# Kernel optimization log

Hardware: AMD Instinct MI355X
Metric: run time of the kernel (lower is better)

## Reference

```python
import jax, jax.numpy as jnp
import numpy as np

N_NODES = 50000
N_EDGES = 800000
F_IN = 512
H1 = 64
H2 = 128
N_CLASSES = 10
N_GRAPHS = 64


def _sage_conv(x, src, dst, w_l, b_l, w_r, n_nodes):
    # mean-aggregate neighbor features (messages flow src -> dst), then
    # out = lin_l(mean_neigh) + lin_r(x)   (PyG SAGEConv defaults)
    msg = x[src]                                           # [E, F] gather
    agg = jax.ops.segment_sum(msg, dst, num_segments=n_nodes)
    deg = jax.ops.segment_sum(jnp.ones((src.shape[0], 1), x.dtype), dst,
                              num_segments=n_nodes)
    mean = agg / jnp.maximum(deg, 1.0)                     # 0 for isolated nodes
    return mean @ w_l + b_l + x @ w_r


def setup_inputs() -> dict:
    key = jax.random.key(0)
    ks = jax.random.split(key, 12)
    x = jax.random.normal(ks[0], (N_NODES, F_IN), dtype=jnp.float32)
    edge_index = jax.random.randint(ks[1], (2, N_EDGES), 0, N_NODES, dtype=jnp.int64)
    batch = jnp.sort(jax.random.randint(ks[2], (N_NODES,), 0, N_GRAPHS, dtype=jnp.int64))

    def glorot(k, fan_in, fan_out):
        s = jnp.sqrt(6.0 / (fan_in + fan_out)).astype(jnp.float32)
        return jax.random.uniform(k, (fan_in, fan_out), jnp.float32, -s, s)

    return {
        "x": x, "edge_index": edge_index, "batch": batch,
        "w1_l": glorot(ks[3], F_IN, H1), "b1_l": jnp.zeros((H1,), jnp.float32),
        "w1_r": glorot(ks[4], F_IN, H1),
        "w2_l": glorot(ks[5], H1, H2), "b2_l": jnp.zeros((H2,), jnp.float32),
        "w2_r": glorot(ks[6], H1, H2),
        "w_fc": glorot(ks[7], H2, N_CLASSES),
        "b_fc": jnp.zeros((N_CLASSES,), jnp.float32),
    }


def reference(x, edge_index, batch, w1_l, b1_l, w1_r, w2_l, b2_l, w2_r, w_fc, b_fc):
    src, dst = edge_index[0], edge_index[1]
    n = x.shape[0]
    h = jax.nn.relu(_sage_conv(x, src, dst, w1_l, b1_l, w1_r, n))
    # dropout is identity in eval mode
    h = _sage_conv(h, src, dst, w2_l, b2_l, w2_r, n)        # [N, H2]
    # global mean pool over graphs
    summed = jax.ops.segment_sum(h, batch, num_segments=N_GRAPHS)
    cnt = jax.ops.segment_sum(jnp.ones((n, 1), h.dtype), batch, num_segments=N_GRAPHS)
    pooled = summed / jnp.maximum(cnt, 1.0)                 # [G, H2]
    logits = pooled @ w_fc + b_fc                           # [G, C]
    return jax.nn.log_softmax(logits, axis=1)
```

## Files before the change

kernel.cpp:

```cpp
#include <hip/hip_runtime.h>

#define NN 50000
#define NE 800000
#define FIN 512
#define H1DIM 64
#define H2DIM 128
#define NC 10
#define NG 64
#define NRT 3125
#define SCAN_BLOCKS 196
#define SLICES 8
#define SLICE_NODES (NN / SLICES)
#define SCAT_GRPS 98
#define SCAT_BLOCKS (SLICES * SCAT_GRPS)

typedef __attribute__((ext_vector_type(8))) short bf16x8;
typedef __attribute__((ext_vector_type(4))) float f32x4;

__device__ inline short f2bf(float f) {
  unsigned u = __float_as_uint(f);
  unsigned r = u + 0x7fffu + ((u >> 16) & 1u);
  return (short)(r >> 16);
}
__device__ inline short f2bf_fast(float f) {
  return (short)((__float_as_uint(f) + 0x8000u) >> 16);
}
__device__ inline float bf2f(short s) {
  return __uint_as_float(((unsigned)(unsigned short)s) << 16);
}

__global__ __launch_bounds__(256) void hist_kernel(const int* __restrict__ dst,
                                                   int* __restrict__ cnt) {
  int i = (blockIdx.x * 256 + threadIdx.x) * 4;
  if (i < NE) {
    int4 d = *(const int4*)(dst + i);
    atomicAdd(&cnt[d.x], 1);
    atomicAdd(&cnt[d.y], 1);
    atomicAdd(&cnt[d.z], 1);
    atomicAdd(&cnt[d.w], 1);
  }
}

__global__ __launch_bounds__(256) void scan1_kernel(const int* __restrict__ cnt,
                                                    int* __restrict__ excl,
                                                    int* __restrict__ bsum) {
  __shared__ int s[256];
  int t = threadIdx.x;
  int i = blockIdx.x * 256 + t;
  int v = (i < NN) ? cnt[i] : 0;
  s[t] = v;
  __syncthreads();
  for (int off = 1; off < 256; off <<= 1) {
    int u = (t >= off) ? s[t - off] : 0;
    __syncthreads();
    s[t] += u;
    __syncthreads();
  }
  if (i < NN) excl[i] = s[t] - v;
  if (t == 255) bsum[blockIdx.x] = s[255];
}

__global__ __launch_bounds__(256) void scan23_kernel(const int* __restrict__ bsum,
                                                     int* __restrict__ rowptr,
                                                     int* __restrict__ cursor) {
  __shared__ int s[256];
  int t = threadIdx.x;
  int b = blockIdx.x;
  int v = (t < SCAN_BLOCKS) ? bsum[t] : 0;
  s[t] = v;
  __syncthreads();
  for (int off = 1; off < 256; off <<= 1) {
    int u = (t >= off) ? s[t - off] : 0;
    __syncthreads();
    s[t] += u;
    __syncthreads();
  }
  int prefix = (b == 0) ? 0 : s[b - 1];
  int i = b * 256 + t;
  if (i < NN) {
    int p = rowptr[i] + prefix;
    rowptr[i] = p;
    cursor[i] = p;
  }
  if (i == 0) rowptr[NN] = NE;
}

__global__ __launch_bounds__(256) void scatter_kernel(
    const int* __restrict__ src, const int* __restrict__ dst,
    int* __restrict__ cursor, int* __restrict__ ssrc) {
  int slice = blockIdx.x & 7;
  int lo = slice * SLICE_NODES;
  int hi = lo + SLICE_NODES;
  int tid = (blockIdx.x >> 3) * 256 + threadIdx.x;
  for (int j = tid; j < NE / 4; j += SCAT_GRPS * 256) {
    int4 s = *(const int4*)(src + j * 4);
    int4 d = *(const int4*)(dst + j * 4);
    if (d.x >= lo && d.x < hi) { int p = atomicAdd(&cursor[d.x], 1); ssrc[p] = s.x; }
    if (d.y >= lo && d.y < hi) { int p = atomicAdd(&cursor[d.y], 1); ssrc[p] = s.y; }
    if (d.z >= lo && d.z < hi) { int p = atomicAdd(&cursor[d.z], 1); ssrc[p] = s.z; }
    if (d.w >= lo && d.w < hi) { int p = atomicAdd(&cursor[d.w], 1); ssrc[p] = s.w; }
  }
}

__global__ __launch_bounds__(256) void wbtf_prep_kernel(
    const float* __restrict__ wl, const float* __restrict__ wr,
    short* __restrict__ wbtf) {
  int w = blockIdx.x * 4 + (threadIdx.x >> 6);
  int lane = threadIdx.x & 63;
  int ni = w >> 4;
  int ks = w & 15;
  int n = ni * 16 + (lane & 15);
  int k = ks * 32 + (lane >> 4) * 8;
  bf16x8 o;
#pragma unroll
  for (int j = 0; j < 8; j++) {
    float v = (n < 64) ? wl[(size_t)(k + j) * 64 + n]
                       : wr[(size_t)(k + j) * 64 + (n - 64)];
    o[j] = f2bf(v);
  }
  *(bf16x8*)(wbtf + ((size_t)w * 64 + lane) * 8) = o;
}

__global__ __launch_bounds__(256) void gemm1_kernel(
    const float* __restrict__ x, const short* __restrict__ wbtf,
    short* __restrict__ xwl, float* __restrict__ xwr) {
  __shared__ short Bs[32768];

  const int t = threadIdx.x;
  const int w = blockIdx.x * 4 + (t >> 6);
  const int wc = (w < NRT) ? w : (NRT - 1);
  const int lane = t & 63;
  const int l15 = lane & 15;
  const int q = lane >> 4;
  const float* px = x + (size_t)(wc * 16 + l15) * FIN + q * 8;

  const f32x4 z = {0.f, 0.f, 0.f, 0.f};
  f32x4 acc[8];
#pragma unroll
  for (int ni = 0; ni < 8; ni++) acc[ni] = z;

  float4 ra0[4], ra1[4];
#pragma unroll
  for (int i = 0; i < 4; i++) {
    ra0[i] = *(const float4*)(px + i * 32);
    ra1[i] = *(const float4*)(px + i * 32 + 4);
  }

#pragma unroll
  for (int h = 0; h < 2; h++) {
    if (h > 0) __syncthreads();
#pragma unroll
    for (int i = 0; i < 16; i++) {
      int c = i * 256 + t;
      int ni = c >> 9;
      int rem = c & 511;
      ((bf16x8*)Bs)[c] =
          *(const bf16x8*)(wbtf + (size_t)ni * 8192 + h * 4096 + rem * 8);
    }
    __syncthreads();

#pragma unroll
    for (int ksl = 0; ksl < 8; ksl++) {
      int ks = h * 8 + ksl;
      int slot = ks & 3;
      bf16x8 af;
      {
        float4 v0 = ra0[slot], v1 = ra1[slot];
        af[0] = f2bf_fast(v0.x); af[1] = f2bf_fast(v0.y);
        af[2] = f2bf_fast(v0.z); af[3] = f2bf_fast(v0.w);
        af[4] = f2bf_fast(v1.x); af[5] = f2bf_fast(v1.y);
        af[6] = f2bf_fast(v1.z); af[7] = f2bf_fast(v1.w);
      }
      if (ks + 4 < 16) {
        ra0[slot] = *(const float4*)(px + (ks + 4) * 32);
        ra1[slot] = *(const float4*)(px + (ks + 4) * 32 + 4);
      }
#pragma unroll
      for (int ni = 0; ni < 8; ni++) {
        bf16x8 bf = *(const bf16x8*)(&Bs[((ni * 8 + ksl) * 64 + lane) * 8]);
        acc[ni] = __builtin_amdgcn_mfma_f32_16x16x32_bf16(af, bf, acc[ni], 0, 0, 0);
      }
    }
  }

  int row_base = wc * 16 + q * 4;
#pragma unroll
  for (int ni = 0; ni < 8; ni++) {
    int col = ni * 16 + l15;
    int c = col & 63;
#pragma unroll
    for (int r = 0; r < 4; r++) {
      int row = row_base + r;
      if (col < 64) xwl[(size_t)row * 64 + c] = f2bf(acc[ni][r]);
      else          xwr[(size_t)row * 64 + c] = acc[ni][r];
    }
  }
}

__global__ __launch_bounds__(256) void agg1_h1_kernel(
    const int* __restrict__ rowptr, const int* __restrict__ ssrc,
    const short* __restrict__ xwl, const float* __restrict__ xwr,
    const float* __restrict__ b1, short* __restrict__ h1) {
  int node = blockIdx.x * 4 + (threadIdx.x >> 6);
  if (node >= NN) return;
  int lane = threadIdx.x & 63;
  int c = lane & 7;
  int r = lane >> 3;
  int lo = rowptr[node], hi = rowptr[node + 1];
  float acc[8];
#pragma unroll
  for (int k = 0; k < 8; k++) acc[k] = 0.f;
  for (int e = lo + r; e < hi; e += 8) {
    int s = ssrc[e];
    bf16x8 v = *(const bf16x8*)(xwl + (size_t)s * 64 + c * 8);
#pragma unroll
    for (int k = 0; k < 8; k++) acc[k] += bf2f(v[k]);
  }
#pragma unroll
  for (int k = 0; k < 8; k++) {
    acc[k] += __shfl_xor(acc[k], 8);
    acc[k] += __shfl_xor(acc[k], 16);
    acc[k] += __shfl_xor(acc[k], 32);
  }
  if (r == 0) {
    float dg = fmaxf((float)(hi - lo), 1.0f);
    const float* xr = xwr + (size_t)node * 64 + c * 8;
    bf16x8 out;
#pragma unroll
    for (int k = 0; k < 8; k++) {
      float v = fmaxf(acc[k] / dg + b1[c * 8 + k] + xr[k], 0.f);
      out[k] = f2bf(v);
    }
    *(bf16x8*)(h1 + (size_t)node * 64 + c * 8) = out;
  }
}

__global__ __launch_bounds__(256) void agg2_kernel(
    const int* __restrict__ rowptr, const int* __restrict__ ssrc,
    const short* __restrict__ h1, float* __restrict__ agg2) {
  int node = blockIdx.x * 4 + (threadIdx.x >> 6);
  if (node >= NN) return;
  int lane = threadIdx.x & 63;
  int c = lane & 7;
  int r = lane >> 3;
  int lo = rowptr[node], hi = rowptr[node + 1];
  float acc[8];
#pragma unroll
  for (int k = 0; k < 8; k++) acc[k] = 0.f;
  for (int e = lo + r; e < hi; e += 8) {
    int s = ssrc[e];
    bf16x8 v = *(const bf16x8*)(h1 + (size_t)s * 64 + c * 8);
#pragma unroll
    for (int k = 0; k < 8; k++) acc[k] += bf2f(v[k]);
  }
#pragma unroll
  for (int k = 0; k < 8; k++) {
    acc[k] += __shfl_xor(acc[k], 8);
    acc[k] += __shfl_xor(acc[k], 16);
    acc[k] += __shfl_xor(acc[k], 32);
  }
  if (r == 0) {
    float* p = agg2 + (size_t)node * 64 + c * 8;
    f32x4 lo4 = {acc[0], acc[1], acc[2], acc[3]};
    f32x4 hi4 = {acc[4], acc[5], acc[6], acc[7]};
    *(f32x4*)(p) = lo4;
    *(f32x4*)(p + 4) = hi4;
  }
}

__global__ __launch_bounds__(256) void pool1_kernel(
    const int* __restrict__ batch, const float* __restrict__ agg2,
    const short* __restrict__ h1, const int* __restrict__ rowptr,
    float* __restrict__ poolA, float* __restrict__ poolB,
    float* __restrict__ poolCnt) {
  int t = threadIdx.x;
  int c = t & 15;
  int s = t >> 4;
  int n0 = blockIdx.x * 256 + s * 16;
  int n1 = n0 + 16;
  if (n1 > NN) n1 = NN;

  f32x4 aA = {0.f, 0.f, 0.f, 0.f};
  f32x4 aB = {0.f, 0.f, 0.f, 0.f};
  int cur_g = -1;
  float run = 0.f;
  for (int n = n0; n < n1; n++) {
    int g = batch[n];
    if (g != cur_g) {
      if (cur_g >= 0) {
        float* pa = poolA + (size_t)cur_g * 64 + c * 4;
        float* pb = poolB + (size_t)cur_g * 64 + c * 4;
#pragma unroll
        for (int k = 0; k < 4; k++) {
          atomicAdd(&pa[k], aA[k]);
          atomicAdd(&pb[k], aB[k]);
        }
        if (c == 0) atomicAdd(&poolCnt[cur_g], run);
      }
      cur_g = g;
      aA = (f32x4){0.f, 0.f, 0.f, 0.f};
      aB = (f32x4){0.f, 0.f, 0.f, 0.f};
      run = 0.f;
    }
    float rd = 1.0f / fmaxf((float)(rowptr[n + 1] - rowptr[n]), 1.0f);
    f32x4 a2 = *(const f32x4*)(agg2 + (size_t)n * 64 + c * 4);
    const short* hp = h1 + (size_t)n * 64 + c * 4;
#pragma unroll
    for (int k = 0; k < 4; k++) {
      aA[k] = fmaf(a2[k], rd, aA[k]);
      aB[k] += bf2f(hp[k]);
    }
    run += 1.f;
  }
  if (cur_g >= 0) {
    float* pa = poolA + (size_t)cur_g * 64 + c * 4;
    float* pb = poolB + (size_t)cur_g * 64 + c * 4;
#pragma unroll
    for (int k = 0; k < 4; k++) {
      atomicAdd(&pa[k], aA[k]);
      atomicAdd(&pb[k], aB[k]);
    }
    if (c == 0) atomicAdd(&poolCnt[cur_g], run);
  }
}

__global__ __launch_bounds__(128) void final_kernel(
    const float* __restrict__ poolA, const float* __restrict__ poolB,
    const float* __restrict__ poolCnt, const float* __restrict__ w2l,
    const float* __restrict__ w2r, const float* __restrict__ b2,
    const float* __restrict__ wfc, const float* __restrict__ bfc,
    float* __restrict__ out) {
  int g = blockIdx.x;
  int j = threadIdx.x;
  __shared__ float sp[H2DIM];
  __shared__ float sl[NC];

  float invc = 1.0f / fmaxf(poolCnt[g], 1.0f);
  float v = b2[j];
  for (int k = 0; k < 64; k++) {
    float a = poolA[g * 64 + k] * invc;
    float b = poolB[g * 64 + k] * invc;
    v = fmaf(a, w2l[k * 128 + j], v);
    v = fmaf(b, w2r[k * 128 + j], v);
  }
  sp[j] = v;
  __syncthreads();
  if (j < NC) {
    float lg = bfc[j];
    for (int k = 0; k < H2DIM; k++) lg = fmaf(sp[k], wfc[k * NC + j], lg);
    sl[j] = lg;
  }
  __syncthreads();
  if (j < NC) {
    float m = -1e30f;
    for (int k = 0; k < NC; k++) m = fmaxf(m, sl[k]);
    float s = 0.f;
    for (int k = 0; k < NC; k++) s += expf(sl[k] - m);
    out[g * NC + j] = sl[j] - m - logf(s);
  }
}

extern "C" void kernel_launch(void* const* d_in, const int* in_sizes, int n_in,
                              void* d_out, int out_size, void* d_ws,
                              size_t ws_size, hipStream_t stream) {
  const float* x   = (const float*)d_in[0];
  const int* edge  = (const int*)d_in[1];
  const int* batch = (const int*)d_in[2];
  const float* w1l = (const float*)d_in[3];
  const float* b1l = (const float*)d_in[4];
  const float* w1r = (const float*)d_in[5];
  const float* w2l = (const float*)d_in[6];
  const float* b2l = (const float*)d_in[7];
  const float* w2r = (const float*)d_in[8];
  const float* wfc = (const float*)d_in[9];
  const float* bfc = (const float*)d_in[10];
  float* out = (float*)d_out;

  const int* src = edge;
  const int* dst = edge + NE;

  const size_t NF = (size_t)NN * 64;
  int*   cnt     = (int*)d_ws;
  float* poolA   = (float*)(cnt + NN);
  float* poolB   = poolA + (size_t)NG * 64;
  float* poolCnt = poolB + (size_t)NG * 64;
  int*   cursor  = (int*)(poolCnt + NG);
  int*   rowptr  = cursor + NN;
  int*   bsum    = rowptr + 50004;
  int*   ssrc    = bsum + 256;
  short* xwl     = (short*)(ssrc + NE);
  short* h1s     = xwl + NF;
  short* wbtf    = h1s + NF;
  float* xwr     = (float*)(wbtf + 65536);
  float* agg2    = xwr + NF;

  hipMemsetAsync(cnt, 0, (NN + 2 * NG * 64 + NG) * sizeof(int), stream);

  hist_kernel<<<(NE / 4 + 255) / 256, 256, 0, stream>>>(dst, cnt);
  scan1_kernel<<<SCAN_BLOCKS, 256, 0, stream>>>(cnt, rowptr, bsum);
  scan23_kernel<<<SCAN_BLOCKS, 256, 0, stream>>>(bsum, rowptr, cursor);
  scatter_kernel<<<SCAT_BLOCKS, 256, 0, stream>>>(src, dst, cursor, ssrc);

  wbtf_prep_kernel<<<32, 256, 0, stream>>>(w1l, w1r, wbtf);
  gemm1_kernel<<<(NRT + 3) / 4, 256, 0, stream>>>(x, wbtf, xwl, xwr);

  agg1_h1_kernel<<<(NN + 3) / 4, 256, 0, stream>>>(rowptr, ssrc, xwl, xwr, b1l, h1s);
  agg2_kernel<<<(NN + 3) / 4, 256, 0, stream>>>(rowptr, ssrc, h1s, agg2);
  pool1_kernel<<<SCAN_BLOCKS, 256, 0, stream>>>(batch, agg2, h1s, rowptr, poolA, poolB, poolCnt);
  final_kernel<<<NG, 128, 0, stream>>>(poolA, poolB, poolCnt, w2l, w2r, b2l, wfc, bfc, out);
}
```

Baseline: 351.3 us.

## Merge independent kernels into horizontally fused launches to overlap scatter with GEMM

Folds the weight-prep kernel into the histogram launch as extra blocks, and merges the CSR scatter with the first GEMM into one launch whose blocks branch by block index. The aim is to cut launch count and let the latency-bound atomic scatter overlap with the compute-bound GEMM on the same device. In exchange, scatter blocks now reserve the GEMM's 64KB of shared memory, which may reduce how many scatter blocks fit on a CU at once.

```diff
diff --git a/kernel.cpp b/kernel.cpp
--- a/kernel.cpp
+++ b/kernel.cpp
@@ -13,6 +13,8 @@
 #define SLICE_NODES (NN / SLICES)
 #define SCAT_GRPS 98
 #define SCAT_BLOCKS (SLICES * SCAT_GRPS)
+#define HIST_BLOCKS 782
+#define GEMM_BLOCKS 782
 
 typedef __attribute__((ext_vector_type(8))) short bf16x8;
 typedef __attribute__((ext_vector_type(4))) float f32x4;
@@ -29,15 +31,35 @@
   return __uint_as_float(((unsigned)(unsigned short)s) << 16);
 }
 
-__global__ __launch_bounds__(256) void hist_kernel(const int* __restrict__ dst,
-                                                   int* __restrict__ cnt) {
-  int i = (blockIdx.x * 256 + threadIdx.x) * 4;
-  if (i < NE) {
-    int4 d = *(const int4*)(dst + i);
-    atomicAdd(&cnt[d.x], 1);
-    atomicAdd(&cnt[d.y], 1);
-    atomicAdd(&cnt[d.z], 1);
-    atomicAdd(&cnt[d.w], 1);
+__global__ __launch_bounds__(256) void histwbtf_kernel(
+    const int* __restrict__ dst, int* __restrict__ cnt,
+    const float* __restrict__ wl, const float* __restrict__ wr,
+    short* __restrict__ wbtf) {
+  int b = blockIdx.x;
+  if (b < HIST_BLOCKS) {
+    int i = (b * 256 + threadIdx.x) * 4;
+    if (i < NE) {
+      int4 d = *(const int4*)(dst + i);
+      atomicAdd(&cnt[d.x], 1);
+      atomicAdd(&cnt[d.y], 1);
+      atomicAdd(&cnt[d.z], 1);
+      atomicAdd(&cnt[d.w], 1);
+    }
+  } else {
+    int w = (b - HIST_BLOCKS) * 4 + (threadIdx.x >> 6);
+    int lane = threadIdx.x & 63;
+    int ni = w >> 4;
+    int ks = w & 15;
+    int n = ni * 16 + (lane & 15);
+    int k = ks * 32 + (lane >> 4) * 8;
+    bf16x8 o;
+#pragma unroll
+    for (int j = 0; j < 8; j++) {
+      float v = (n < 64) ? wl[(size_t)(k + j) * 64 + n]
+                         : wr[(size_t)(k + j) * 64 + (n - 64)];
+      o[j] = f2bf(v);
+    }
+    *(bf16x8*)(wbtf + ((size_t)w * 64 + lane) * 8) = o;
   }
 }
 
@@ -85,49 +107,31 @@
   if (i == 0) rowptr[NN] = NE;
 }
 
-__global__ __launch_bounds__(256) void scatter_kernel(
+__global__ __launch_bounds__(256) void scatgemm_kernel(
     const int* __restrict__ src, const int* __restrict__ dst,
-    int* __restrict__ cursor, int* __restrict__ ssrc) {
-  int slice = blockIdx.x & 7;
-  int lo = slice * SLICE_NODES;
-  int hi = lo + SLICE_NODES;
-  int tid = (blockIdx.x >> 3) * 256 + threadIdx.x;
-  for (int j = tid; j < NE / 4; j += SCAT_GRPS * 256) {
-    int4 s = *(const int4*)(src + j * 4);
-    int4 d = *(const int4*)(dst + j * 4);
-    if (d.x >= lo && d.x < hi) { int p = atomicAdd(&cursor[d.x], 1); ssrc[p] = s.x; }
-    if (d.y >= lo && d.y < hi) { int p = atomicAdd(&cursor[d.y], 1); ssrc[p] = s.y; }
-    if (d.z >= lo && d.z < hi) { int p = atomicAdd(&cursor[d.z], 1); ssrc[p] = s.z; }
-    if (d.w >= lo && d.w < hi) { int p = atomicAdd(&cursor[d.w], 1); ssrc[p] = s.w; }
-  }
-}
-
-__global__ __launch_bounds__(256) void wbtf_prep_kernel(
-    const float* __restrict__ wl, const float* __restrict__ wr,
-    short* __restrict__ wbtf) {
-  int w = blockIdx.x * 4 + (threadIdx.x >> 6);
-  int lane = threadIdx.x & 63;
-  int ni = w >> 4;
-  int ks = w & 15;
-  int n = ni * 16 + (lane & 15);
-  int k = ks * 32 + (lane >> 4) * 8;
-  bf16x8 o;
-#pragma unroll
-  for (int j = 0; j < 8; j++) {
-    float v = (n < 64) ? wl[(size_t)(k + j) * 64 + n]
-                       : wr[(size_t)(k + j) * 64 + (n - 64)];
-    o[j] = f2bf(v);
-  }
-  *(bf16x8*)(wbtf + ((size_t)w * 64 + lane) * 8) = o;
-}
-
-__global__ __launch_bounds__(256) void gemm1_kernel(
+    int* __restrict__ cursor, int* __restrict__ ssrc,
     const float* __restrict__ x, const short* __restrict__ wbtf,
     short* __restrict__ xwl, float* __restrict__ xwr) {
   __shared__ short Bs[32768];
 
+  if (blockIdx.x < SCAT_BLOCKS) {
+    int slice = blockIdx.x & 7;
+    int lo = slice * SLICE_NODES;
+    int hi = lo + SLICE_NODES;
+    int tid = (blockIdx.x >> 3) * 256 + threadIdx.x;
+    for (int j = tid; j < NE / 4; j += SCAT_GRPS * 256) {
+      int4 s = *(const int4*)(src + j * 4);
+      int4 d = *(const int4*)(dst + j * 4);
+      if (d.x >= lo && d.x < hi) { int p = atomicAdd(&cursor[d.x], 1); ssrc[p] = s.x; }
+      if (d.y >= lo && d.y < hi) { int p = atomicAdd(&cursor[d.y], 1); ssrc[p] = s.y; }
+      if (d.z >= lo && d.z < hi) { int p = atomicAdd(&cursor[d.z], 1); ssrc[p] = s.z; }
+      if (d.w >= lo && d.w < hi) { int p = atomicAdd(&cursor[d.w], 1); ssrc[p] = s.w; }
+    }
+    return;
+  }
+
   const int t = threadIdx.x;
-  const int w = blockIdx.x * 4 + (t >> 6);
+  const int w = (blockIdx.x - SCAT_BLOCKS) * 4 + (t >> 6);
   const int wc = (w < NRT) ? w : (NRT - 1);
   const int lane = t & 63;
   const int l15 = lane & 15;
@@ -396,13 +400,11 @@
 
   hipMemsetAsync(cnt, 0, (NN + 2 * NG * 64 + NG) * sizeof(int), stream);
 
-  hist_kernel<<<(NE / 4 + 255) / 256, 256, 0, stream>>>(dst, cnt);
+  histwbtf_kernel<<<HIST_BLOCKS + 32, 256, 0, stream>>>(dst, cnt, w1l, w1r, wbtf);
   scan1_kernel<<<SCAN_BLOCKS, 256, 0, stream>>>(cnt, rowptr, bsum);
   scan23_kernel<<<SCAN_BLOCKS, 256, 0, stream>>>(bsum, rowptr, cursor);
-  scatter_kernel<<<SCAT_BLOCKS, 256, 0, stream>>>(src, dst, cursor, ssrc);
-
-  wbtf_prep_kernel<<<32, 256, 0, stream>>>(w1l, w1r, wbtf);
-  gemm1_kernel<<<(NRT + 3) / 4, 256, 0, stream>>>(x, wbtf, xwl, xwr);
+  scatgemm_kernel<<<SCAT_BLOCKS + GEMM_BLOCKS, 256, 0, stream>>>(
+      src, dst, cursor, ssrc, x, wbtf, xwl, xwr);
 
   agg1_h1_kernel<<<(NN + 3) / 4, 256, 0, stream>>>(rowptr, ssrc, xwl, xwr, b1l, h1s);
   agg2_kernel<<<(NN + 3) / 4, 256, 0, stream>>>(rowptr, ssrc, h1s, agg2);
```

Measured after the change: 347.0 us. No clear change (-1.2%).
